# Kernel optimization log

Measured on AMD Instinct MI355X. Metric: run time of the kernel, lower is better.

The kernel has to match this reference:

```python
import jax, jax.numpy as jnp
import numpy as np

B, S = 128, 128
AH, VH, TH = 64, 64, 128  # audio/vision/text LSTM hidden sizes
FUSED = (AH + 1) * (VH + 1) * (TH + 1)  # 545025
PF = 128  # post_fusion_dim


def setup_inputs() -> dict:
    key = jax.random.key(0)
    ks = jax.random.split(key, 6)
    return {
        "audio_h": jax.random.normal(ks[0], (B, S, AH), jnp.float32),
        "vision_h": jax.random.normal(ks[1], (B, S, VH), jnp.float32),
        "text_h": jax.random.normal(ks[2], (B, S, TH), jnp.float32),
        "W1": jax.random.normal(ks[3], (PF, FUSED), jnp.float32) * 0.001,
        "b1": jnp.zeros((PF,), jnp.float32),
        "W2": jax.random.normal(ks[4], (PF, PF), jnp.float32) * 0.05,
        "b2": jnp.zeros((PF,), jnp.float32),
        "W3": jax.random.normal(ks[5], (1, PF), jnp.float32) * 0.05,
        "b3": jnp.zeros((1,), jnp.float32),
    }


def reference(audio_h, vision_h, text_h, W1, b1, W2, b2, W3, b3):
    b, s = audio_h.shape[0], audio_h.shape[1]
    ones = jnp.ones((b, s, 1), audio_h.dtype)
    a = jnp.concatenate([ones, audio_h], axis=2)   # [B,S,AH+1]
    v = jnp.concatenate([ones, vision_h], axis=2)  # [B,S,VH+1]
    t = jnp.concatenate([ones, text_h], axis=2)    # [B,S,TH+1]
    # sum_t outer(a_t, v_t, t_t): one fused contraction over the time axis
    fusion = jnp.einsum('bsa,bsv,bsw->bavw', a, v, t)  # [B,AH+1,VH+1,TH+1]
    fusion = fusion.reshape(b, -1)                      # matches torch view order (a,v,t)
    # T2FN low-rank regularizer scale
    tmp = jnp.sqrt(jnp.asarray(AH * VH * TH / max(AH, VH, TH), jnp.float32))
    # post-fusion MLP (dropout p=0 -> identity)
    y1 = jax.nn.relu(fusion @ W1.T + b1)
    y2 = jax.nn.relu(y1 @ W2.T + b2)
    out = y2 @ W3.T + b3  # [B,1]
    out = jax.nn.sigmoid(out) * 6.0 - 3.0  # output_range=6, output_shift=-3
    norm = jnp.linalg.norm(fusion, axis=1)  # [B]
    reg_loss = jnp.mean(tmp * norm)
    return (out, reg_loss)
```

## Files before the change

### kernel.cpp

```cpp
#include <hip/hip_runtime.h>
#include <math.h>

#define BB 128
#define SS 128
#define AE 65
#define VE 65
#define TE 129
#define PFD 128
#define FUSED 545025UL
#define FUSEDI 545025
#define VSTRIDE 136
#define APLANE 8840
#define FPP 574976UL
#define FPPI 574976
#define KSP 512
#define NBLK 1123
#define NST 8

typedef _Float16 half4 __attribute__((ext_vector_type(4)));
typedef _Float16 half8 __attribute__((ext_vector_type(8)));
typedef float f32x16 __attribute__((ext_vector_type(16)));

__device__ __forceinline__ void gll16(const void* g, void* l) {
  __builtin_amdgcn_global_load_lds((const __attribute__((address_space(1))) void*)g,
                                   (__attribute__((address_space(3))) void*)l, 16, 0, 0);
}

__global__ __launch_bounds__(256) void k_initf(_Float16* __restrict__ Fh,
                                               float* __restrict__ y1pre,
                                               float* __restrict__ normsq,
                                               float* __restrict__ Flast) {
  const int b = blockIdx.x;
  const int tid = threadIdx.x;
  _Float16* base = Fh + (size_t)b * FPP;
  for (int i = tid; i < 29575; i += 256) {
    const int a = i / 455, r = i - a * 455;
    const int v = r / 7, e = r - v * 7;
    base[a * APLANE + v * VSTRIDE + 129 + e] = (_Float16)0.f;
  }
  for (int i = tid; i < 376; i += 256) base[574600 + i] = (_Float16)0.f;
  if (tid < PFD) y1pre[b * PFD + tid] = 0.f;
  if (tid == 128) normsq[b] = 0.f;
  if (tid == 129) Flast[b] = 0.f;
}

__global__ __launch_bounds__(256) void k_core(
    const float* __restrict__ audio, const float* __restrict__ vision,
    const float* __restrict__ text, _Float16* __restrict__ Fh,
    float* __restrict__ normsq)
{
  const int b  = blockIdx.x;
  const int gy = blockIdx.y;
  const int gz = blockIdx.z;
  const int tid = threadIdx.x;
  const int wv = tid >> 6, ln = tid & 63;
  const int lr = ln & 31, hb = ln >> 5;

  __shared__ float    sVt[64][132];
  __shared__ float    sAc[8][132];
  __shared__ _Float16 sTh[64][136];
  __shared__ _Float16 sTl[64][136];

  {
    const float* vb = vision + (size_t)b * SS * 64;
#pragma unroll
    for (int r = 0; r < 32; ++r) {
      const int e = tid + 256 * r;
      sVt[e & 63][e >> 6] = vb[e];
    }
    const float* ab = audio + (size_t)b * SS * 64 + 8 * gy;
#pragma unroll
    for (int r = 0; r < 4; ++r) {
      const int e = tid + 256 * r;
      sAc[e & 7][e >> 3] = ab[(e >> 3) * 64 + (e & 7)];
    }
    const int wbase = 64 * gz;
    const float* tb = text + (size_t)b * SS * 128;
#pragma unroll
    for (int r = 0; r < 32; ++r) {
      const int e = tid + 256 * r;
      const int s = e >> 6, wl = e & 63;
      const int w = wbase + wl;
      const float val = (w == 0) ? 1.f : tb[s * 128 + w - 1];
      const _Float16 th = (_Float16)val;
      sTh[wl][s] = th;
      sTl[wl][s] = (_Float16)((val - (float)th) * 2048.f);
    }
  }
  __syncthreads();

  float ss = 0.f;
  for (int i = 0; i < 8; ++i) {
    const int u  = 8 * wv + i;
    const int rt = u >> 1, wt = u & 1;
    const int j  = rt >> 1, vh = rt & 1;
    const int v0m = 32 * vh;
    const int wl0 = 32 * wt;

    f32x16 acc = {}, accl = {};
#pragma unroll
    for (int ks = 0; ks < 8; ++ks) {
      const int s0 = 16 * ks + 8 * hb;
      const float4 x0 = *(const float4*)&sVt[v0m + lr][s0];
      const float4 x1 = *(const float4*)&sVt[v0m + lr][s0 + 4];
      const float4 a0 = *(const float4*)&sAc[j][s0];
      const float4 a1 = *(const float4*)&sAc[j][s0 + 4];
      const float pp[8] = {a0.x * x0.x, a0.y * x0.y, a0.z * x0.z, a0.w * x0.w,
                           a1.x * x1.x, a1.y * x1.y, a1.z * x1.z, a1.w * x1.w};
      half8 afh, afl;
#pragma unroll
      for (int e = 0; e < 8; ++e) {
        const _Float16 h = (_Float16)pp[e];
        afh[e] = h;
        afl[e] = (_Float16)((pp[e] - (float)h) * 2048.f);
      }
      const half8 bqh = *(const half8*)&sTh[wl0 + lr][s0];
      const half8 bql = *(const half8*)&sTl[wl0 + lr][s0];
      acc  = __builtin_amdgcn_mfma_f32_32x32x16_f16(afh, bqh, acc,  0, 0, 0);
      accl = __builtin_amdgcn_mfma_f32_32x32x16_f16(afl, bqh, accl, 0, 0, 0);
      accl = __builtin_amdgcn_mfma_f32_32x32x16_f16(afh, bql, accl, 0, 0, 0);
    }

    const int a = 1 + 8 * gy + j;
    _Float16* Fb = Fh + (size_t)b * FPP + (size_t)a * APLANE;
    const int wg = 64 * gz + wl0 + lr;
#pragma unroll
    for (int reg = 0; reg < 16; ++reg) {
      const int crow = (reg & 3) + 8 * (reg >> 2) + 4 * hb;
      const int v = 1 + 32 * vh + crow;
      const float f = acc[reg] + accl[reg] * (1.f / 2048.f);
      ss += f * f;
      Fb[(size_t)v * VSTRIDE + wg] = (_Float16)f;
    }
  }

#pragma unroll
  for (int off = 32; off > 0; off >>= 1) ss += __shfl_down(ss, off);
  if (ln == 0) atomicAdd(&normsq[b], ss);
}

__global__ __launch_bounds__(256) void k_planes(
    const float* __restrict__ audio, const float* __restrict__ vision,
    const float* __restrict__ text, _Float16* __restrict__ Fh,
    float* __restrict__ Flast, float* __restrict__ normsq)
{
  const int b = blockIdx.x;
  const int which = blockIdx.y;
  const int tid = threadIdx.x;
  const int tw = tid & 15, tv = tid >> 4;
  __shared__ __align__(16) char smem[28800];

  float ss = 0.f;

  if (which == 0) {
    float (*sv)[80]  = (float(*)[80])smem;
    float (*st)[144] = (float(*)[144])(smem + 10240);
    float acc[5][9];
#pragma unroll
    for (int i = 0; i < 5; ++i)
#pragma unroll
      for (int j = 0; j < 9; ++j) acc[i][j] = 0.f;

    for (int c = 0; c < 4; ++c) {
      const int s0 = 32 * c;
      __syncthreads();
      const float* vbase = &vision[((size_t)(b * SS + s0)) * 64];
#pragma unroll
      for (int r = 0; r < 8; ++r) {
        const int e = tid + 256 * r;
        sv[e >> 6][(e & 63) + 1] = vbase[e];
      }
      const float* tbase = &text[((size_t)(b * SS + s0)) * 128];
#pragma unroll
      for (int r = 0; r < 16; ++r) {
        const int e = tid + 256 * r;
        st[e >> 7][(e & 127) + 1] = tbase[e];
      }
      if (tid < 32) { sv[tid][0] = 1.f; st[tid][0] = 1.f; }
      __syncthreads();
      for (int s = 0; s < 32; ++s) {
        float vr[5], tr[9];
#pragma unroll
        for (int i = 0; i < 5; ++i) {
          const int vx = tv + 16 * i;
          vr[i] = (vx < VE) ? sv[s][vx] : 0.f;
        }
#pragma unroll
        for (int j = 0; j < 9; ++j) {
          const int wx = tw + 16 * j;
          tr[j] = (wx < TE) ? st[s][wx] : 0.f;
        }
#pragma unroll
        for (int i = 0; i < 5; ++i)
#pragma unroll
          for (int j = 0; j < 9; ++j) acc[i][j] += vr[i] * tr[j];
      }
    }
    _Float16* Fb = Fh + (size_t)b * FPP;
#pragma unroll
    for (int i = 0; i < 5; ++i) {
      const int v = tv + 16 * i;
      if (v < VE) {
#pragma unroll
        for (int j = 0; j < 9; ++j) {
          const int w = tw + 16 * j;
          if (w < TE) {
            const float m = acc[i][j];
            Fb[(size_t)v * VSTRIDE + w] = (_Float16)m;
            ss += m * m;
          }
        }
      }
    }
  } else if (which == 1) {
    float (*sa)[64]  = (float(*)[64])smem;
    float (*st)[144] = (float(*)[144])(smem + 10240);
    float acc[4][9];
#pragma unroll
    for (int i = 0; i < 4; ++i)
#pragma unroll
      for (int j = 0; j < 9; ++j) acc[i][j] = 0.f;

    for (int c = 0; c < 4; ++c) {
      const int s0 = 32 * c;
      __syncthreads();
      const float* abase = &audio[((size_t)(b * SS + s0)) * 64];
#pragma unroll
      for (int r = 0; r < 8; ++r) {
        const int e = tid + 256 * r;
        sa[e >> 6][e & 63] = abase[e];
      }
      const float* tbase = &text[((size_t)(b * SS + s0)) * 128];
#pragma unroll
      for (int r = 0; r < 16; ++r) {
        const int e = tid + 256 * r;
        st[e >> 7][(e & 127) + 1] = tbase[e];
      }
      if (tid < 32) st[tid][0] = 1.f;
      __syncthreads();
      for (int s = 0; s < 32; ++s) {
        float ar[4], tr[9];
#pragma unroll
        for (int i = 0; i < 4; ++i) ar[i] = sa[s][tv + 16 * i];
#pragma unroll
        for (int j = 0; j < 9; ++j) {
          const int wx = tw + 16 * j;
          tr[j] = (wx < TE) ? st[s][wx] : 0.f;
        }
#pragma unroll
        for (int i = 0; i < 4; ++i)
#pragma unroll
          for (int j = 0; j < 9; ++j) acc[i][j] += ar[i] * tr[j];
      }
    }
#pragma unroll
    for (int i = 0; i < 4; ++i) {
      const int a = 1 + tv + 16 * i;
      _Float16* Fb = Fh + (size_t)b * FPP + (size_t)a * APLANE;
#pragma unroll
      for (int j = 0; j < 9; ++j) {
        const int w = tw + 16 * j;
        if (w < TE) {
          const float m = acc[i][j];
          Fb[w] = (_Float16)m;
          ss += m * m;
        }
      }
    }
  } else {
    float (*sa)[64] = (float(*)[64])smem;
    float (*sv)[64] = (float(*)[64])(smem + 10240);
    float* swt = (float*)(smem + 10240 + 8192);
    float acc[4][4];
#pragma unroll
    for (int i = 0; i < 4; ++i)
#pragma unroll
      for (int j = 0; j < 4; ++j) acc[i][j] = 0.f;

    for (int c = 0; c < 4; ++c) {
      const int s0 = 32 * c;
      __syncthreads();
      const float* abase = &audio[((size_t)(b * SS + s0)) * 64];
      const float* vbase = &vision[((size_t)(b * SS + s0)) * 64];
#pragma unroll
      for (int r = 0; r < 8; ++r) {
        const int e = tid + 256 * r;
        sa[e >> 6][e & 63] = abase[e];
        sv[e >> 6][e & 63] = vbase[e];
      }
      if (tid < 32) swt[tid] = text[((size_t)(b * SS + s0 + tid)) * 128 + 127];
      __syncthreads();
      for (int s = 0; s < 32; ++s) {
        const float t = swt[s];
        float ar[4], vr[4];
#pragma unroll
        for (int i = 0; i < 4; ++i) ar[i] = sa[s][tv + 16 * i] * t;
#pragma unroll
        for (int j = 0; j < 4; ++j) vr[j] = sv[s][tw + 16 * j];
#pragma unroll
        for (int i = 0; i < 4; ++i)
#pragma unroll
          for (int j = 0; j < 4; ++j) acc[i][j] += ar[i] * vr[j];
      }
    }
#pragma unroll
    for (int i = 0; i < 4; ++i) {
      const int a = 1 + tv + 16 * i;
      _Float16* Fb = Fh + (size_t)b * FPP + (size_t)a * APLANE;
#pragma unroll
      for (int j = 0; j < 4; ++j) {
        const int v = 1 + tw + 16 * j;
        float m = acc[i][j];
        ss += m * m;
        if (a == 64 && v == 64) { Flast[b] = m; m = 0.f; }
        Fb[(size_t)v * VSTRIDE + 128] = (_Float16)m;
      }
    }
  }

#pragma unroll
  for (int off = 32; off > 0; off >>= 1) ss += __shfl_down(ss, off);
  if ((tid & 63) == 0) atomicAdd(&normsq[b], ss);
}

__global__ __launch_bounds__(256) void k_gemm(
    const float* __restrict__ W1, const _Float16* __restrict__ Fh,
    float* __restrict__ parts)
{
  __shared__ _Float16 sB[2][8192];
  __shared__ _Float16 sA[4][2048];

  const int tid = threadIdx.x;
  const int wv = tid >> 6, ln = tid & 63;
  const int lb = ln & 31, hb = ln >> 5;
  const int kp0 = blockIdx.x * KSP;

  const int loff = (ln & 15) << 2;
  int wtr, kot;
  {
    const int kpl = kp0 + loff;
    const int a = kpl / APLANE;
    const int rem = kpl - a * APLANE;
    const int v = rem / VSTRIDE;
    wtr = rem - v * VSTRIDE;
    kot = a * 8385 + v * 129 + wtr;
  }
  const float* wbase = W1 + (size_t)((wv << 5) + (ln >> 4)) * FUSED;

  const int brow = (wv << 5) + (ln >> 3);
  const int sslot = (ln & 7) ^ ((ln >> 3) & 7);
  const _Float16* FhB = Fh + (size_t)brow * FPP + kp0 + (sslot << 3);

  f32x16 acc0 = {}, acc1 = {}, acc2 = {}, acc3 = {};
  float4 xa[8];

#define LOADA                                                              \
  {                                                                        \
    const int kc = (kot <= 545021) ? kot : 545021;                         \
    _Pragma("unroll")                                                      \
    for (int n = 0; n < 8; ++n)                                            \
      __builtin_memcpy(&xa[n], wbase + (size_t)(4 * n) * FUSED + kc, 16);  \
    wtr += 64;                                                             \
    if (wtr >= VSTRIDE) { wtr -= VSTRIDE; kot += 57; } else kot += 64;     \
  }

#define WRITEA                                                             \
  {                                                                        \
    _Pragma("unroll")                                                      \
    for (int n = 0; n < 8; ++n) {                                          \
      const int Rl = 4 * n + (ln >> 4);                                    \
      const int sp = (((ln & 15) >> 1) ^ (Rl & 7));                        \
      half4 h;                                                             \
      h[0] = (_Float16)xa[n].x; h[1] = (_Float16)xa[n].y;                  \
      h[2] = (_Float16)xa[n].z; h[3] = (_Float16)xa[n].w;                  \
      *(half4*)((char*)&sA[wv][0] + (Rl << 7) + (sp << 4) + ((ln & 1) << 3)) = h; \
    }                                                                      \
  }

#define STAGEB(BUF, KOFF)                                                  \
  {                                                                        \
    _Pragma("unroll")                                                      \
    for (int n = 0; n < 4; ++n) {                                          \
      gll16(FhB + (size_t)(n << 3) * FPP + (KOFF),                         \
            (char*)&sB[BUF][0] + (((wv << 5) + (n << 3)) << 7));           \
    }                                                                      \
  }

  LOADA
  STAGEB(0, 0)
  __syncthreads();

  int buf = 0;
  for (int t = 0; t < NST; ++t) {
    WRITEA
    if (t + 1 < NST) {
      LOADA
      STAGEB(buf ^ 1, (t + 1) * 64)
    }
    const _Float16* sBb = &sB[buf][0];
    const char* sAw = (const char*)&sA[wv][0] + (lb << 7);
#pragma unroll
    for (int j = 0; j < 4; ++j) {
      const half8 af = *(const half8*)(sAw + ((((j << 1) + hb) ^ (lb & 7)) << 4));
      const int slot = ((j << 1) + hb) ^ (lb & 7);
      const char* bbase = (const char*)sBb + (lb << 7) + (slot << 4);
      const half8 b0 = *(const half8*)(bbase);
      const half8 b1 = *(const half8*)(bbase + 4096);
      const half8 b2 = *(const half8*)(bbase + 8192);
      const half8 b3 = *(const half8*)(bbase + 12288);
      acc0 = __builtin_amdgcn_mfma_f32_32x32x16_f16(af, b0, acc0, 0, 0, 0);
      acc1 = __builtin_amdgcn_mfma_f32_32x32x16_f16(af, b1, acc1, 0, 0, 0);
      acc2 = __builtin_amdgcn_mfma_f32_32x32x16_f16(af, b2, acc2, 0, 0, 0);
      acc3 = __builtin_amdgcn_mfma_f32_32x32x16_f16(af, b3, acc3, 0, 0, 0);
    }
    __syncthreads();
    buf ^= 1;
  }
#undef LOADA
#undef WRITEA
#undef STAGEB

  f32x16* o = (f32x16*)(parts + ((size_t)blockIdx.x * 256 + tid) * 64);
  o[0] = acc0; o[1] = acc1; o[2] = acc2; o[3] = acc3;
}

__global__ __launch_bounds__(256) void k_red(const float* __restrict__ parts,
                                             float* __restrict__ y1pre)
{
  const int tid = threadIdx.x;
  const int T = blockIdx.x * 4 + (tid >> 6);
  const int R = tid & 63;
  float s = 0.f;
  for (int sl = blockIdx.y; sl < NBLK; sl += 16)
    s += parts[(size_t)sl * 16384 + T * 64 + R];
  const int wv2 = T >> 6, hb2 = (T >> 5) & 1, lb2 = T & 31;
  const int q = R >> 4, rg = R & 15;
  const int b = q * 32 + lb2;
  const int pp = wv2 * 32 + (rg & 3) + 8 * (rg >> 2) + 4 * hb2;
  atomicAdd(&y1pre[b * PFD + pp], s);
}

__global__ __launch_bounds__(128) void k_final(
    const float* __restrict__ y1pre, const float* __restrict__ b1,
    const float* __restrict__ W2, const float* __restrict__ b2,
    const float* __restrict__ W3, const float* __restrict__ b3,
    const float* __restrict__ W1, const float* __restrict__ Flast,
    const float* __restrict__ normsq, float* __restrict__ out)
{
  const int b = blockIdx.x, p = threadIdx.x;
  __shared__ float y1[PFD];
  __shared__ float red[PFD];
  const float extra = W1[(size_t)p * FUSED + (FUSED - 1)] * Flast[b];
  y1[p] = fmaxf(y1pre[(size_t)b * PFD + p] + extra + b1[p], 0.f);
  __syncthreads();
  float s = b2[p];
  for (int k = 0; k < PFD; ++k) s += y1[k] * W2[p * PFD + k];
  const float y2 = fmaxf(s, 0.f);
  red[p] = y2 * W3[p];
  __syncthreads();
  for (int off = 64; off > 0; off >>= 1) {
    if (p < off) red[p] += red[p + off];
    __syncthreads();
  }
  if (p == 0) {
    const float x = red[0] + b3[0];
    out[b] = 6.f / (1.f + expf(-x)) - 3.f;
  }
  if (b == 0) {
    __syncthreads();
    red[p] = sqrtf(normsq[p]);
    __syncthreads();
    for (int off = 64; off > 0; off >>= 1) {
      if (p < off) red[p] += red[p + off];
      __syncthreads();
    }
    if (p == 0) out[BB] = 64.f * red[0] / (float)BB;
  }
}

extern "C" void kernel_launch(void* const* d_in, const int* in_sizes, int n_in,
                              void* d_out, int out_size, void* d_ws, size_t ws_size,
                              hipStream_t stream) {
  const float* audio  = (const float*)d_in[0];
  const float* vision = (const float*)d_in[1];
  const float* text   = (const float*)d_in[2];
  const float* W1     = (const float*)d_in[3];
  const float* b1     = (const float*)d_in[4];
  const float* W2     = (const float*)d_in[5];
  const float* b2     = (const float*)d_in[6];
  const float* W3     = (const float*)d_in[7];
  const float* b3     = (const float*)d_in[8];
  float* out = (float*)d_out;

  float* y1pre  = (float*)d_ws;
  float* normsq = y1pre + BB * PFD;
  float* Flast  = normsq + BB;
  _Float16* Fh  = (_Float16*)((char*)d_ws + 131072);
  float* parts  = (float*)((char*)d_ws + 147324928);

  k_initf<<<BB, 256, 0, stream>>>(Fh, y1pre, normsq, Flast);

  k_core<<<dim3(BB, 8, 2), 256, 0, stream>>>(audio, vision, text, Fh, normsq);
  k_planes<<<dim3(BB, 3), 256, 0, stream>>>(audio, vision, text, Fh, Flast, normsq);

  k_gemm<<<NBLK, 256, 0, stream>>>(W1, Fh, parts);
  k_red<<<dim3(64, 16), 256, 0, stream>>>(parts, y1pre);

  k_final<<<BB, PFD, 0, stream>>>(y1pre, b1, W2, b2, W3, b3, W1, Flast, normsq, out);
}
```

Baseline: 314.2 us.

## Triple-buffer k_gemm with smaller K steps and explicit vmcnt waits

Rewrites the split-K GEMM main loop to stage the F operand through three LDS buffers with K steps of 32 instead of two buffers with K steps of 64. The 16 steps are fully unrolled, and each uses a single barrier preceded by a hand-placed s_waitcnt vmcnt. This lets two B tiles plus the next W1 register prefetch stay in flight while the MFMAs run. The intent is to hide global-load latency better and shrink LDS use, possibly helping occupancy. The cost is more barriers and half-sized per-step work, and correctness now depends on the manual vmcnt accounting.

Result: slower. 334.5 us (+6.5%).

```diff
diff --git a/kernel.cpp b/kernel.cpp
--- a/kernel.cpp
+++ b/kernel.cpp
@@ -15,7 +15,6 @@
 #define FPPI 574976
 #define KSP 512
 #define NBLK 1123
-#define NST 8
 
 typedef _Float16 half4 __attribute__((ext_vector_type(4)));
 typedef _Float16 half8 __attribute__((ext_vector_type(8)));
@@ -327,95 +326,125 @@
     const float* __restrict__ W1, const _Float16* __restrict__ Fh,
     float* __restrict__ parts)
 {
-  __shared__ _Float16 sB[2][8192];
-  __shared__ _Float16 sA[4][2048];
+  __shared__ _Float16 sB3[3][4096];
+  __shared__ _Float16 sA[4][1024];
 
   const int tid = threadIdx.x;
   const int wv = tid >> 6, ln = tid & 63;
   const int lb = ln & 31, hb = ln >> 5;
   const int kp0 = blockIdx.x * KSP;
 
-  const int loff = (ln & 15) << 2;
   int wtr, kot;
   {
-    const int kpl = kp0 + loff;
+    const int kpl = kp0 + ((ln & 7) << 2);
     const int a = kpl / APLANE;
     const int rem = kpl - a * APLANE;
     const int v = rem / VSTRIDE;
     wtr = rem - v * VSTRIDE;
     kot = a * 8385 + v * 129 + wtr;
   }
-  const float* wbase = W1 + (size_t)((wv << 5) + (ln >> 4)) * FUSED;
-
-  const int brow = (wv << 5) + (ln >> 3);
-  const int sslot = (ln & 7) ^ ((ln >> 3) & 7);
-  const _Float16* FhB = Fh + (size_t)brow * FPP + kp0 + (sslot << 3);
+  const float* wbase = W1 + (size_t)((wv << 5) + (ln >> 3)) * FUSED;
+
+  const int brow0 = (wv << 5) + (ln >> 2);
+  const int slogB = (ln & 3) ^ ((ln >> 2) & 3);
+  const _Float16* FhP0 = Fh + (size_t)brow0 * FPP + kp0 + (slogB << 3);
+  const _Float16* FhP1 = FhP0 + (size_t)16 * FPP;
 
   f32x16 acc0 = {}, acc1 = {}, acc2 = {}, acc3 = {};
-  float4 xa[8];
+  float4 xa[4];
 
 #define LOADA                                                              \
   {                                                                        \
     const int kc = (kot <= 545021) ? kot : 545021;                         \
     _Pragma("unroll")                                                      \
-    for (int n = 0; n < 8; ++n)                                            \
-      __builtin_memcpy(&xa[n], wbase + (size_t)(4 * n) * FUSED + kc, 16);  \
-    wtr += 64;                                                             \
-    if (wtr >= VSTRIDE) { wtr -= VSTRIDE; kot += 57; } else kot += 64;     \
+    for (int n = 0; n < 4; ++n)                                            \
+      __builtin_memcpy(&xa[n], wbase + (size_t)(8 * n) * FUSED + kc, 16);  \
+    wtr += 32;                                                             \
+    if (wtr >= VSTRIDE) { wtr -= VSTRIDE; kot += 25; } else kot += 32;     \
   }
 
 #define WRITEA                                                             \
   {                                                                        \
     _Pragma("unroll")                                                      \
-    for (int n = 0; n < 8; ++n) {                                          \
-      const int Rl = 4 * n + (ln >> 4);                                    \
-      const int sp = (((ln & 15) >> 1) ^ (Rl & 7));                        \
+    for (int n = 0; n < 4; ++n) {                                          \
+      const int Rl = 8 * n + (ln >> 3);                                    \
+      const int sp = (((ln & 7) >> 1) ^ (Rl & 3));                         \
       half4 h;                                                             \
       h[0] = (_Float16)xa[n].x; h[1] = (_Float16)xa[n].y;                  \
       h[2] = (_Float16)xa[n].z; h[3] = (_Float16)xa[n].w;                  \
-      *(half4*)((char*)&sA[wv][0] + (Rl << 7) + (sp << 4) + ((ln & 1) << 3)) = h; \
+      *(half4*)((char*)&sA[wv][0] + (Rl << 6) + (sp << 4) + ((ln & 1) << 3)) = h; \
     }                                                                      \
   }
 
 #define STAGEB(BUF, KOFF)                                                  \
   {                                                                        \
-    _Pragma("unroll")                                                      \
-    for (int n = 0; n < 4; ++n) {                                          \
-      gll16(FhB + (size_t)(n << 3) * FPP + (KOFF),                         \
-            (char*)&sB[BUF][0] + (((wv << 5) + (n << 3)) << 7));           \
-    }                                                                      \
-  }
-
+    gll16(FhP0 + (KOFF), (char*)&sB3[BUF][0] + ((wv << 5) << 6));          \
+    gll16(FhP1 + (KOFF), (char*)&sB3[BUF][0] + (((wv << 5) + 16) << 6));   \
+  }
+
+#define GSTEP(T, WSTR)                                                         \
+  {                                                                            \
+    asm volatile("s_waitcnt " WSTR ::: "memory");                              \
+    __builtin_amdgcn_sched_barrier(0);                                         \
+    __builtin_amdgcn_s_barrier();                                              \
+    __builtin_amdgcn_sched_barrier(0);                                         \
+    WRITEA                                                                     \
+    if ((T) + 1 < 16) { LOADA }                                                \
+    if ((T) + 2 < 16) { STAGEB(((T) + 2) % 3, ((T) + 2) * 32) }                \
+    __builtin_amdgcn_sched_barrier(0);                                         \
+    {                                                                          \
+      const _Float16* sBb = &sB3[(T) % 3][0];                                  \
+      const char* sAw = (const char*)&sA[wv][0] + (lb << 6);                   \
+      {                                                                        \
+        const int sl = hb;                                                     \
+        const half8 af = *(const half8*)(sAw + ((sl ^ (lb & 3)) << 4));        \
+        const char* bbase = (const char*)sBb + (lb << 6) + ((sl ^ (lb & 3)) << 4); \
+        const half8 b0 = *(const half8*)(bbase);                               \
+        const half8 b1 = *(const half8*)(bbase + 2048);                        \
+        const half8 b2 = *(const half8*)(bbase + 4096);                        \
+        const half8 b3 = *(const half8*)(bbase + 6144);                        \
+        acc0 = __builtin_amdgcn_mfma_f32_32x32x16_f16(af, b0, acc0, 0, 0, 0);  \
+        acc1 = __builtin_amdgcn_mfma_f32_32x32x16_f16(af, b1, acc1, 0, 0, 0);  \
+        acc2 = __builtin_amdgcn_mfma_f32_32x32x16_f16(af, b2, acc2, 0, 0, 0);  \
+        acc3 = __builtin_amdgcn_mfma_f32_32x32x16_f16(af, b3, acc3, 0, 0, 0);  \
+      }                                                                        \
+      {                                                                        \
+        const int sl = 2 + hb;                                                 \
+        const half8 af = *(const half8*)(sAw + ((sl ^ (lb & 3)) << 4));        \
+        const char* bbase = (const char*)sBb + (lb << 6) + ((sl ^ (lb & 3)) << 4); \
+        const half8 b0 = *(const half8*)(bbase);                               \
+        const half8 b1 = *(const half8*)(bbase + 2048);                        \
+        const half8 b2 = *(const half8*)(bbase + 4096);                        \
+        const half8 b3 = *(const half8*)(bbase + 6144);                        \
+        acc0 = __builtin_amdgcn_mfma_f32_32x32x16_f16(af, b0, acc0, 0, 0, 0);  \
+        acc1 = __builtin_amdgcn_mfma_f32_32x32x16_f16(af, b1, acc1, 0, 0, 0);  \
+        acc2 = __builtin_amdgcn_mfma_f32_32x32x16_f16(af, b2, acc2, 0, 0, 0);  \
+        acc3 = __builtin_amdgcn_mfma_f32_32x32x16_f16(af, b3, acc3, 0, 0, 0);  \
+      }                                                                        \
+    }                                                                          \
+  }
+
+  STAGEB(0, 0)
   LOADA
-  STAGEB(0, 0)
-  __syncthreads();
-
-  int buf = 0;
-  for (int t = 0; t < NST; ++t) {
-    WRITEA
-    if (t + 1 < NST) {
-      LOADA
-      STAGEB(buf ^ 1, (t + 1) * 64)
-    }
-    const _Float16* sBb = &sB[buf][0];
-    const char* sAw = (const char*)&sA[wv][0] + (lb << 7);
-#pragma unroll
-    for (int j = 0; j < 4; ++j) {
-      const half8 af = *(const half8*)(sAw + ((((j << 1) + hb) ^ (lb & 7)) << 4));
-      const int slot = ((j << 1) + hb) ^ (lb & 7);
-      const char* bbase = (const char*)sBb + (lb << 7) + (slot << 4);
-      const half8 b0 = *(const half8*)(bbase);
-      const half8 b1 = *(const half8*)(bbase + 4096);
-      const half8 b2 = *(const half8*)(bbase + 8192);
-      const half8 b3 = *(const half8*)(bbase + 12288);
-      acc0 = __builtin_amdgcn_mfma_f32_32x32x16_f16(af, b0, acc0, 0, 0, 0);
-      acc1 = __builtin_amdgcn_mfma_f32_32x32x16_f16(af, b1, acc1, 0, 0, 0);
-      acc2 = __builtin_amdgcn_mfma_f32_32x32x16_f16(af, b2, acc2, 0, 0, 0);
-      acc3 = __builtin_amdgcn_mfma_f32_32x32x16_f16(af, b3, acc3, 0, 0, 0);
-    }
-    __syncthreads();
-    buf ^= 1;
-  }
+  STAGEB(1, 32)
+
+  GSTEP(0,  "vmcnt(2)")
+  GSTEP(1,  "vmcnt(2)")
+  GSTEP(2,  "vmcnt(2)")
+  GSTEP(3,  "vmcnt(2)")
+  GSTEP(4,  "vmcnt(2)")
+  GSTEP(5,  "vmcnt(2)")
+  GSTEP(6,  "vmcnt(2)")
+  GSTEP(7,  "vmcnt(2)")
+  GSTEP(8,  "vmcnt(2)")
+  GSTEP(9,  "vmcnt(2)")
+  GSTEP(10, "vmcnt(2)")
+  GSTEP(11, "vmcnt(2)")
+  GSTEP(12, "vmcnt(2)")
+  GSTEP(13, "vmcnt(2)")
+  GSTEP(14, "vmcnt(2)")
+  GSTEP(15, "vmcnt(0)")
+#undef GSTEP
 #undef LOADA
 #undef WRITEA
 #undef STAGEB
```

## Double-buffer W1 register prefetch with manual vmcnt waits and one barrier per step

Applied to the files above, without the earlier changes.

The main fused-GEMM loop is fully unrolled into eight explicit steps. W1 tiles now alternate between two register buffers, so global loads are issued two stages ahead. The two __syncthreads per iteration become a single s_barrier, guarded by an explicit s_waitcnt vmcnt and sched_barriers, so that only the needed loads are drained before each step. This aims to hide more of the HBM latency of streaming the huge W1 matrix, at the cost of extra VGPRs and fragile hand-counted waitcnt values.

Result: no change. 316.7 us (+0.8%).

```diff
diff --git a/kernel.cpp b/kernel.cpp
--- a/kernel.cpp
+++ b/kernel.cpp
@@ -352,27 +352,27 @@
   const _Float16* FhB = Fh + (size_t)brow * FPP + kp0 + (sslot << 3);
 
   f32x16 acc0 = {}, acc1 = {}, acc2 = {}, acc3 = {};
-  float4 xa[8];
-
-#define LOADA                                                              \
+  float4 xaP[8], xaQ[8];
+
+#define LOADA(S)                                                           \
   {                                                                        \
     const int kc = (kot <= 545021) ? kot : 545021;                         \
     _Pragma("unroll")                                                      \
     for (int n = 0; n < 8; ++n)                                            \
-      __builtin_memcpy(&xa[n], wbase + (size_t)(4 * n) * FUSED + kc, 16);  \
+      __builtin_memcpy(&xa##S[n], wbase + (size_t)(4 * n) * FUSED + kc, 16); \
     wtr += 64;                                                             \
     if (wtr >= VSTRIDE) { wtr -= VSTRIDE; kot += 57; } else kot += 64;     \
   }
 
-#define WRITEA                                                             \
+#define WRITEA(S)                                                          \
   {                                                                        \
     _Pragma("unroll")                                                      \
     for (int n = 0; n < 8; ++n) {                                          \
       const int Rl = 4 * n + (ln >> 4);                                    \
       const int sp = (((ln & 15) >> 1) ^ (Rl & 7));                        \
       half4 h;                                                             \
-      h[0] = (_Float16)xa[n].x; h[1] = (_Float16)xa[n].y;                  \
-      h[2] = (_Float16)xa[n].z; h[3] = (_Float16)xa[n].w;                  \
+      h[0] = (_Float16)xa##S[n].x; h[1] = (_Float16)xa##S[n].y;            \
+      h[2] = (_Float16)xa##S[n].z; h[3] = (_Float16)xa##S[n].w;            \
       *(half4*)((char*)&sA[wv][0] + (Rl << 7) + (sp << 4) + ((ln & 1) << 3)) = h; \
     }                                                                      \
   }
@@ -386,36 +386,49 @@
     }                                                                      \
   }
 
-  LOADA
+#define GSTEP(T, S, WSTR)                                                      \
+  {                                                                            \
+    asm volatile("s_waitcnt " WSTR ::: "memory");                              \
+    __builtin_amdgcn_sched_barrier(0);                                         \
+    __builtin_amdgcn_s_barrier();                                              \
+    __builtin_amdgcn_sched_barrier(0);                                         \
+    WRITEA(S)                              \
+    if ((T) + 1 < NST) { STAGEB(((T) + 1) & 1, ((T) + 1) * 64) }               \
+    if ((T) + 2 < NST) { LOADA(S) }          \
+    __builtin_amdgcn_sched_barrier(0);                                         \
+    {                                                                          \
+      const _Float16* sBb = &sB[(T) & 1][0];                                   \
+      const char* sAw = (const char*)&sA[wv][0] + (lb << 7);                   \
+      _Pragma("unroll")                                                        \
+      for (int j = 0; j < 4; ++j) {                                            \
+        const half8 af = *(const half8*)(sAw + ((((j << 1) + hb) ^ (lb & 7)) << 4)); \
+        const int slot = ((j << 1) + hb) ^ (lb & 7);                           \
+        const char* bbase = (const char*)sBb + (lb << 7) + (slot << 4);        \
+        const half8 b0 = *(const half8*)(bbase);                               \
+        const half8 b1 = *(const half8*)(bbase + 4096);                        \
+        const half8 b2 = *(const half8*)(bbase + 8192);                        \
+        const half8 b3 = *(const half8*)(bbase + 12288);                       \
+        acc0 = __builtin_amdgcn_mfma_f32_32x32x16_f16(af, b0, acc0, 0, 0, 0);  \
+        acc1 = __builtin_amdgcn_mfma_f32_32x32x16_f16(af, b1, acc1, 0, 0, 0);  \
+        acc2 = __builtin_amdgcn_mfma_f32_32x32x16_f16(af, b2, acc2, 0, 0, 0);  \
+        acc3 = __builtin_amdgcn_mfma_f32_32x32x16_f16(af, b3, acc3, 0, 0, 0);  \
+      }                                                                        \
+    }                                                                          \
+  }
+
+  LOADA(P)
   STAGEB(0, 0)
-  __syncthreads();
-
-  int buf = 0;
-  for (int t = 0; t < NST; ++t) {
-    WRITEA
-    if (t + 1 < NST) {
-      LOADA
-      STAGEB(buf ^ 1, (t + 1) * 64)
-    }
-    const _Float16* sBb = &sB[buf][0];
-    const char* sAw = (const char*)&sA[wv][0] + (lb << 7);
-#pragma unroll
-    for (int j = 0; j < 4; ++j) {
-      const half8 af = *(const half8*)(sAw + ((((j << 1) + hb) ^ (lb & 7)) << 4));
-      const int slot = ((j << 1) + hb) ^ (lb & 7);
-      const char* bbase = (const char*)sBb + (lb << 7) + (slot << 4);
-      const half8 b0 = *(const half8*)(bbase);
-      const half8 b1 = *(const half8*)(bbase + 4096);
-      const half8 b2 = *(const half8*)(bbase + 8192);
-      const half8 b3 = *(const half8*)(bbase + 12288);
-      acc0 = __builtin_amdgcn_mfma_f32_32x32x16_f16(af, b0, acc0, 0, 0, 0);
-      acc1 = __builtin_amdgcn_mfma_f32_32x32x16_f16(af, b1, acc1, 0, 0, 0);
-      acc2 = __builtin_amdgcn_mfma_f32_32x32x16_f16(af, b2, acc2, 0, 0, 0);
-      acc3 = __builtin_amdgcn_mfma_f32_32x32x16_f16(af, b3, acc3, 0, 0, 0);
-    }
-    __syncthreads();
-    buf ^= 1;
-  }
+  LOADA(Q)
+
+  GSTEP(0, P, "vmcnt(8)")
+  GSTEP(1, Q, "vmcnt(8)")
+  GSTEP(2, P, "vmcnt(8)")
+  GSTEP(3, Q, "vmcnt(8)")
+  GSTEP(4, P, "vmcnt(8)")
+  GSTEP(5, Q, "vmcnt(8)")
+  GSTEP(6, P, "vmcnt(8)")
+  GSTEP(7, Q, "vmcnt(0)")
+#undef GSTEP
 #undef LOADA
 #undef WRITEA
 #undef STAGEB
```
